# Performance work log

Hardware: AMD Instinct MI355X
Metric: run time of the kernel (lower is better)

## Reference

```python
import jax, jax.numpy as jnp
import numpy as np

B, C, H, W = 16, 64, 128, 128
C8 = C // 8


def setup_inputs() -> dict:
    key = jax.random.key(0)
    ks = jax.random.split(key, 8)
    s = 0.05
    return {
        "x": jax.random.normal(ks[0], (B, C, H, W), dtype=jnp.float32),
        "Wq": jax.random.normal(ks[1], (C8, C), dtype=jnp.float32) * s,
        "bq": jax.random.normal(ks[2], (C8,), dtype=jnp.float32) * s,
        "Wk": jax.random.normal(ks[3], (C8, C), dtype=jnp.float32) * s,
        "bk": jax.random.normal(ks[4], (C8,), dtype=jnp.float32) * s,
        "Wv": jax.random.normal(ks[5], (C, C), dtype=jnp.float32) * s,
        "bv": jax.random.normal(ks[6], (C,), dtype=jnp.float32) * s,
        "gamma": jnp.zeros((1,), dtype=jnp.float32),
    }


def _criss_cross(x, Wq, bq, Wk, bk, Wv, bv, gamma):
    # 1x1 convs == channel-mixing matmuls
    q = jnp.einsum("bchw,oc->bohw", x, Wq) + bq[None, :, None, None]  # [B,C8,H,W]
    k = jnp.einsum("bchw,oc->bohw", x, Wk) + bk[None, :, None, None]  # [B,C8,H,W]
    v = jnp.einsum("bchw,oc->bohw", x, Wv) + bv[None, :, None, None]  # [B,C,H,W]

    h = x.shape[2]
    # column (H-axis) attention scores; diagonal masked to -inf
    energy_H = jnp.einsum("bchw,bciw->bhwi", q, k)  # [B,H,W,H]
    diag = jnp.eye(h, dtype=bool)[None, :, None, :]  # mask where query row == key row
    energy_H = jnp.where(diag, -jnp.inf, energy_H)
    # row (W-axis) attention scores
    energy_W = jnp.einsum("bchw,bchj->bhwj", q, k)  # [B,H,W,W]

    # joint softmax over concatenated H+W axis
    att = jax.nn.softmax(jnp.concatenate([energy_H, energy_W], axis=3), axis=3)
    att_H = att[:, :, :, :h]    # [B,H,W,H]
    att_W = att[:, :, :, h:]    # [B,H,W,W]

    out_H = jnp.einsum("bhwi,bciw->bchw", att_H, v)
    out_W = jnp.einsum("bhwj,bchj->bchw", att_W, v)
    return gamma[0] * (out_H + out_W) + x


def reference(x, Wq, bq, Wk, bk, Wv, bv, gamma):
    return _criss_cross(x, Wq, bq, Wk, bk, Wv, bv, gamma)
```

## Files before the change

### kernel.cpp

```cpp
#include <hip/hip_runtime.h>

#define HW 128
#define CC 64
#define NB 16
#define LOG2E 1.44269504088896f

typedef _Float16 h1;
typedef _Float16 h2 __attribute__((ext_vector_type(2)));
typedef _Float16 half8 __attribute__((ext_vector_type(8)));
typedef float float16v __attribute__((ext_vector_type(16)));
typedef uint uv4 __attribute__((ext_vector_type(4)));

__device__ __forceinline__ uint packh2(float a, float b) {
#if __has_builtin(__builtin_amdgcn_cvt_pkrtz)
  return __builtin_bit_cast(uint, __builtin_amdgcn_cvt_pkrtz(a, b));
#else
  h2 v; v[0] = (h1)a; v[1] = (h1)b; return __builtin_bit_cast(uint, v);
#endif
}
__device__ __forceinline__ ushort f2h(float a) { h1 v = (h1)a; return __builtin_bit_cast(ushort, v); }
__device__ __forceinline__ float  h2f(ushort a) { return (float)__builtin_bit_cast(h1, a); }

__device__ __forceinline__ float fexp2(float x) {
#if __has_builtin(__builtin_amdgcn_exp2f)
  return __builtin_amdgcn_exp2f(x);
#else
  return exp2f(x);
#endif
}

__device__ __forceinline__ float16v mfma16(uv4 a, uv4 b, float16v c) {
  return __builtin_amdgcn_mfma_f32_32x32x16_f16(
      __builtin_bit_cast(half8, a), __builtin_bit_cast(half8, b), c, 0, 0, 0);
}

__global__ __launch_bounds__(256) void k_prep(
    const float* __restrict__ Wq, const float* __restrict__ bq,
    const float* __restrict__ Wk, const float* __restrict__ bk,
    const float* __restrict__ Wv, const float* __restrict__ bv,
    ushort* __restrict__ W_frag, float* __restrict__ bias_f)
{
  int idx = blockIdx.x * 256 + threadIdx.x;
  if (idx < 6144) {
    int g = idx >> 3, e = idx & 7;
    int kshi = g / 96, o = g % 96;
    int ks = kshi >> 1, hi = kshi & 1;
    int c = 8 * hi + 16 * ks + e;
    float val = (o < 8)  ? Wq[o * 64 + c] * LOG2E
              : (o < 16) ? Wk[(o - 8) * 64 + c]
              : (o < 80) ? Wv[(o - 16) * 64 + c] : 0.f;
    W_frag[idx] = f2h(val);
  }
  if (blockIdx.x == 0 && threadIdx.x < 96) {
    int t = threadIdx.x;
    bias_f[t] = (t < 8) ? bq[t] * LOG2E : (t < 16) ? bk[t - 8] : (t < 80) ? bv[t - 16] : 0.f;
  }
}

__global__ __launch_bounds__(256, 4) void k_projW(
    const float* __restrict__ x, const ushort* __restrict__ W_frag,
    const float* __restrict__ bias_f,
    ushort* __restrict__ qT, ushort* __restrict__ kT,
    ushort* __restrict__ v,
    ushort* __restrict__ oW_, float* __restrict__ mW_, float* __restrict__ sW_)
{
  alignas(16) __shared__ uint V_l[64 * 64];
  alignas(16) __shared__ ushort qk_l[128 * 24];
  __shared__ float bias_l[96];

  int t = threadIdx.x;
  int lane = t & 63, wv = t >> 6, hi = lane >> 5;
  int b = blockIdx.x >> 7, r = blockIdx.x & 127;
  if (t < 96) bias_l[t] = bias_f[t];

  int w = 32 * wv + (lane & 31);
  const float* xw = x + (size_t)(b * CC) * (HW * HW) + (size_t)r * HW + w;
  const size_t PL = (size_t)HW * HW;

  float xv[32];
  #pragma unroll
  for (int ks = 0; ks < 4; ++ks) {
    int c0 = 8 * hi + 16 * ks;
    #pragma unroll
    for (int e = 0; e < 8; ++e)
      xv[ks * 8 + e] = xw[(size_t)(c0 + e) * PL];
  }
  __syncthreads();

  float16v acc0 = {}, acc1 = {}, acc2 = {};
  #pragma unroll
  for (int ks = 0; ks < 4; ++ks) {
    uv4 Bx;
    #pragma unroll
    for (int e2 = 0; e2 < 4; ++e2)
      Bx[e2] = packh2(xv[ks * 8 + 2 * e2], xv[ks * 8 + 2 * e2 + 1]);
    const ushort* wf = W_frag + (size_t)(ks * 2 + hi) * 96 * 8;
    uv4 a0 = *(const uv4*)(wf + (lane & 31) * 8);
    uv4 a1 = *(const uv4*)(wf + ((lane & 31) + 32) * 8);
    uv4 a2 = *(const uv4*)(wf + ((lane & 31) + 64) * 8);
    acc0 = mfma16(a0, Bx, acc0);
    acc1 = mfma16(a1, Bx, acc1);
    acc2 = mfma16(a2, Bx, acc2);
  }

  #pragma unroll
  for (int reg = 0; reg < 16; ++reg) {
    int orow = (reg & 3) + 8 * (reg >> 2) + 4 * hi;
    float v0 = acc0[reg] + bias_l[orow];
    if (orow < 16) {
      qk_l[w * 24 + orow] = f2h(v0);
    } else {
      int c = orow - 16;
      *(ushort*)((char*)V_l + c * 256 + ((2 * w) ^ ((c & 15) << 4))) = f2h(v0);
    }
    int c1 = orow + 16;
    *(ushort*)((char*)V_l + c1 * 256 + ((2 * w) ^ ((c1 & 15) << 4))) =
        f2h(acc1[reg] + bias_l[orow + 32]);
    if (orow < 16) {
      int c2_ = orow + 48;
      *(ushort*)((char*)V_l + c2_ * 256 + ((2 * w) ^ ((c2_ & 15) << 4))) =
          f2h(acc2[reg] + bias_l[orow + 64]);
    }
  }
  __syncthreads();

  ushort* vb = v + (size_t)(b * CC) * PL + (size_t)r * HW;
  #pragma unroll
  for (int i = 0; i < 4; ++i) {
    int idx = t + 256 * i; int c = idx >> 4, j8 = idx & 15;
    uv4 val = *(const uv4*)((const char*)V_l + c * 256 + ((16 * j8) ^ ((c & 15) << 4)));
    *(uv4*)(vb + (size_t)c * PL + j8 * 8) = val;
  }
  {
    int pix = t & 127, isk = t >> 7;
    uv4 val = *(const uv4*)&qk_l[pix * 24 + isk * 8];
    ushort* dstt = (isk ? kT : qT) + ((size_t)(b * HW + pix) * HW + r) * 8;
    *(uv4*)dstt = val;
  }

  int qg = w;
  uv4 Bq = {0, 0, 0, 0};
  uv4 ka[4] = {{0,0,0,0}, {0,0,0,0}, {0,0,0,0}, {0,0,0,0}};
  if (hi == 0) {
    Bq = *(const uv4*)&qk_l[qg * 24];
    #pragma unroll
    for (int mt = 0; mt < 4; ++mt)
      ka[mt] = *(const uv4*)&qk_l[((lane & 31) + 32 * mt) * 24 + 8];
  }

  float16v e[4];
  #pragma unroll
  for (int mt = 0; mt < 4; ++mt) {
    float16v z = {};
    e[mt] = mfma16(ka[mt], Bq, z);
  }

  float m = -INFINITY;
  #pragma unroll
  for (int mt = 0; mt < 4; ++mt)
    #pragma unroll
    for (int reg = 0; reg < 16; reg += 2)
      m = fmaxf(m, fmaxf(e[mt][reg], e[mt][reg + 1]));
  m = fmaxf(m, __shfl_xor(m, 32));

  float s0 = 0.f, s1 = 0.f, s2 = 0.f, s3 = 0.f;
  #pragma unroll
  for (int mt = 0; mt < 4; ++mt) {
    #pragma unroll
    for (int reg = 0; reg < 16; reg += 4) {
      float p0 = fexp2(e[mt][reg + 0] - m);
      float p1 = fexp2(e[mt][reg + 1] - m);
      float p2 = fexp2(e[mt][reg + 2] - m);
      float p3 = fexp2(e[mt][reg + 3] - m);
      e[mt][reg + 0] = p0; e[mt][reg + 1] = p1;
      e[mt][reg + 2] = p2; e[mt][reg + 3] = p3;
      s0 += p0; s1 += p1; s2 += p2; s3 += p3;
    }
  }
  float s = (s0 + s1) + (s2 + s3);
  s += __shfl_xor(s, 32);
  if (lane < 32) {
    mW_[(size_t)blockIdx.x * HW + qg] = m;
    sW_[(size_t)blockIdx.x * HW + qg] = s;
  }

  float16v pacc0 = {}, pacc1 = {};
  #pragma unroll
  for (int s8 = 0; s8 < 8; ++s8) {
    int mt = s8 >> 1, hf = s8 & 1;
    float p0 = e[mt][8 * hf + 0], p1 = e[mt][8 * hf + 1];
    float p2 = e[mt][8 * hf + 2], p3 = e[mt][8 * hf + 3];
    float p4 = e[mt][8 * hf + 4], p5 = e[mt][8 * hf + 5];
    float p6 = e[mt][8 * hf + 6], p7 = e[mt][8 * hf + 7];
    uint X = packh2(p0, p1), Y = packh2(p2, p3), Z = packh2(p4, p5), Wp = packh2(p6, p7);
    uint Xs = __shfl_xor(X, 32), Ys = __shfl_xor(Y, 32);
    uint Zs = __shfl_xor(Z, 32), Ws = __shfl_xor(Wp, 32);
    uv4 Bp;
    Bp[0] = (hi == 0) ? X  : Zs;
    Bp[1] = (hi == 0) ? Y  : Ws;
    Bp[2] = (hi == 0) ? Xs : Z;
    Bp[3] = (hi == 0) ? Ys : Wp;
    #pragma unroll
    for (int ct = 0; ct < 2; ++ct) {
      int c = (lane & 31) + 32 * ct;
      uint byteoff = c * 256 + ((16 * (hi + 2 * s8)) ^ ((c & 15) << 4));
      uv4 va = *(const uv4*)((const char*)V_l + byteoff);
      if (ct == 0) pacc0 = mfma16(va, Bp, pacc0);
      else         pacc1 = mfma16(va, Bp, pacc1);
    }
  }

  __syncthreads();
  ushort* o_l = (ushort*)V_l;
  #pragma unroll
  for (int reg = 0; reg < 16; ++reg) {
    int c = (reg & 3) + 8 * (reg >> 2) + 4 * hi;
    o_l[(c +  0) * 128 + w] = f2h(pacc0[reg]);
    o_l[(c + 32) * 128 + w] = f2h(pacc1[reg]);
  }
  __syncthreads();
  ushort* ob = oW_ + (size_t)(b * CC) * PL + (size_t)r * HW;
  #pragma unroll
  for (int i = 0; i < 4; ++i) {
    int idx = t + 256 * i; int c = idx >> 4, w8 = idx & 15;
    *(uv4*)(ob + (size_t)c * PL + w8 * 8) = *(const uv4*)&o_l[c * 128 + w8 * 8];
  }
}

__global__ __launch_bounds__(256) void k_transpose_v(const ushort* __restrict__ v,
                                                     ushort* __restrict__ vT)
{
  __shared__ ushort tl[128 * 130];
  int t = threadIdx.x;
  size_t base = (size_t)blockIdx.x * (HW * HW);
  const uint* ip = (const uint*)(v + base);
  uint* op = (uint*)(vT + base);
  int c2 = t & 63;
  int r0 = t >> 6;
  for (int it = 0; it < 32; ++it) {
    int r = it * 4 + r0;
    uint val = ip[r * 64 + c2];
    *(uint*)&tl[r * 130 + c2 * 2] = val;
  }
  __syncthreads();
  for (int it = 0; it < 32; ++it) {
    int wcol = it * 4 + r0;
    int hh = c2 * 2;
    uint lo = tl[hh * 130 + wcol];
    uint hi = tl[(hh + 1) * 130 + wcol];
    op[wcol * 64 + c2] = lo | (hi << 16);
  }
}

__global__ __launch_bounds__(256, 4) void k_attnH(
    const ushort* __restrict__ qT, const ushort* __restrict__ kT,
    const ushort* __restrict__ vT,
    const float* __restrict__ mW_, const float* __restrict__ sW_,
    ushort* __restrict__ oH_, ushort* __restrict__ aWn)
{
  alignas(16) __shared__ uint V_l[64 * 64];

  int t = threadIdx.x;
  int lane = t & 63, wv = t >> 6;
  int hi = lane >> 5;
  int bid = blockIdx.x;
  int b = bid >> 7, r = bid & 127;
  size_t plane32 = (size_t)(HW * HW) / 2;
  const size_t PL = (size_t)HW * HW;
  size_t pixbase = (size_t)(b * HW + r) * HW * 8;

  int qg = 32 * wv + (lane & 31);
  uv4 Bq = {0, 0, 0, 0};
  uv4 ka[4] = {{0,0,0,0}, {0,0,0,0}, {0,0,0,0}, {0,0,0,0}};
  if (hi == 0) {
    Bq = *(const uv4*)(qT + pixbase + (size_t)qg * 8);
    #pragma unroll
    for (int mt = 0; mt < 4; ++mt)
      ka[mt] = *(const uv4*)(kT + pixbase + (size_t)((lane & 31) + 32 * mt) * 8);
  }
  float mw = mW_[(size_t)b * PL + (size_t)qg * HW + r];
  float sw = sW_[(size_t)b * PL + (size_t)qg * HW + r];

  const uint* vrow = (const uint*)vT + (size_t)(b * CC) * plane32 + (size_t)r * 64;
  #pragma unroll
  for (int i = 0; i < 4; ++i) {
    int idx = t + 256 * i; int c = idx >> 4, j4 = idx & 15;
    uv4 val = *(const uv4*)(vrow + (size_t)c * plane32 + 4 * j4);
    uint byteoff = c * 256 + ((16 * j4) ^ ((c & 15) << 4));
    *(uv4*)((char*)V_l + byteoff) = val;
  }
  __syncthreads();

  float16v e[4];
  #pragma unroll
  for (int mt = 0; mt < 4; ++mt) {
    float16v z = {};
    e[mt] = mfma16(ka[mt], Bq, z);
  }

  #pragma unroll
  for (int mt = 0; mt < 4; ++mt)
    #pragma unroll
    for (int reg = 0; reg < 16; ++reg) {
      int key = 32 * mt + ((reg & 3) + 8 * (reg >> 2) + 4 * hi);
      e[mt][reg] = (key == qg) ? -INFINITY : e[mt][reg];
    }

  float m = -INFINITY;
  #pragma unroll
  for (int mt = 0; mt < 4; ++mt)
    #pragma unroll
    for (int reg = 0; reg < 16; reg += 2)
      m = fmaxf(m, fmaxf(e[mt][reg], e[mt][reg + 1]));
  m = fmaxf(m, __shfl_xor(m, 32));

  float s0 = 0.f, s1 = 0.f, s2 = 0.f, s3 = 0.f;
  #pragma unroll
  for (int mt = 0; mt < 4; ++mt) {
    #pragma unroll
    for (int reg = 0; reg < 16; reg += 4) {
      float p0 = fexp2(e[mt][reg + 0] - m);
      float p1 = fexp2(e[mt][reg + 1] - m);
      float p2 = fexp2(e[mt][reg + 2] - m);
      float p3 = fexp2(e[mt][reg + 3] - m);
      e[mt][reg + 0] = p0; e[mt][reg + 1] = p1;
      e[mt][reg + 2] = p2; e[mt][reg + 3] = p3;
      s0 += p0; s1 += p1; s2 += p2; s3 += p3;
    }
  }
  float s = (s0 + s1) + (s2 + s3);
  s += __shfl_xor(s, 32);

  float mm = fmaxf(m, mw);
  float eh = fexp2(m - mm), ew = fexp2(mw - mm);
  float inv = 1.f / (s * eh + sw * ew);
  float aH = eh * inv;
  if (hi == 0)
    aWn[(size_t)b * PL + (size_t)qg * HW + r] = f2h(ew * inv);

  float16v acc0 = {}, acc1 = {};
  #pragma unroll
  for (int s8 = 0; s8 < 8; ++s8) {
    int mt = s8 >> 1, hf = s8 & 1;
    float p0 = e[mt][8 * hf + 0], p1 = e[mt][8 * hf + 1];
    float p2 = e[mt][8 * hf + 2], p3 = e[mt][8 * hf + 3];
    float p4 = e[mt][8 * hf + 4], p5 = e[mt][8 * hf + 5];
    float p6 = e[mt][8 * hf + 6], p7 = e[mt][8 * hf + 7];
    uint X = packh2(p0, p1), Y = packh2(p2, p3), Z = packh2(p4, p5), Wp = packh2(p6, p7);
    uint Xs = __shfl_xor(X, 32), Ys = __shfl_xor(Y, 32);
    uint Zs = __shfl_xor(Z, 32), Ws = __shfl_xor(Wp, 32);
    uv4 Bp;
    Bp[0] = (hi == 0) ? X  : Zs;
    Bp[1] = (hi == 0) ? Y  : Ws;
    Bp[2] = (hi == 0) ? Xs : Z;
    Bp[3] = (hi == 0) ? Ys : Wp;
    #pragma unroll
    for (int ct = 0; ct < 2; ++ct) {
      int c = (lane & 31) + 32 * ct;
      uint byteoff = c * 256 + ((16 * (hi + 2 * s8)) ^ ((c & 15) << 4));
      uv4 va = *(const uv4*)((const char*)V_l + byteoff);
      if (ct == 0) acc0 = mfma16(va, Bp, acc0);
      else         acc1 = mfma16(va, Bp, acc1);
    }
  }

  __syncthreads();
  ushort* o_l = (ushort*)V_l;
  int w = 32 * wv + (lane & 31);
  #pragma unroll
  for (int reg = 0; reg < 16; ++reg) {
    int c = (reg & 3) + 8 * (reg >> 2) + 4 * hi;
    o_l[(c +  0) * 128 + w] = f2h(acc0[reg] * aH);
    o_l[(c + 32) * 128 + w] = f2h(acc1[reg] * aH);
  }
  __syncthreads();
  ushort* ob = oH_ + (size_t)(b * CC) * PL + (size_t)r * HW;
  #pragma unroll
  for (int i = 0; i < 4; ++i) {
    int idx = t + 256 * i; int c = idx >> 4, w8 = idx & 15;
    *(uv4*)(ob + (size_t)c * PL + w8 * 8) = *(const uv4*)&o_l[c * 128 + w8 * 8];
  }
}

__global__ __launch_bounds__(256) void k_merge(
    const ushort* __restrict__ oHT, const ushort* __restrict__ oW,
    const ushort* __restrict__ aWn,
    const float* __restrict__ x, const float* __restrict__ gamma,
    float* __restrict__ out)
{
  alignas(16) __shared__ ushort otile[2 * 32 * 132];
  int t = threadIdx.x;
  int bid = blockIdx.x;
  int wsel = bid & 3, cg = (bid >> 2) & 31, b = bid >> 7;
  int w0 = wsel * 32;
  float g = gamma[0];
  const int PL = HW * HW;

  uv4 ov[4];
  #pragma unroll
  for (int i = 0; i < 4; ++i) {
    int p = t + 256 * i;
    int ch = p >> 9, rest = p & 511;
    int w = rest >> 4, hg = rest & 15;
    size_t cbase = (size_t)(b * CC + cg * 2 + ch) * PL;
    ov[i] = *(const uv4*)(oHT + cbase + (size_t)(w0 + w) * HW + hg * 8);
  }
  uint2 owp[8]; float4 xp[8]; uint2 awp[4];
  #pragma unroll
  for (int i = 0; i < 2; ++i) {
    int p = t + 256 * i;
    int w4 = p & 7, hh2 = p >> 3;
    #pragma unroll
    for (int rr = 0; rr < 2; ++rr) {
      int hh = 2 * hh2 + rr;
      size_t poff = (size_t)hh * HW + w0 + 4 * w4;
      awp[i * 2 + rr] = *(const uint2*)(aWn + (size_t)b * PL + poff);
      #pragma unroll
      for (int ch = 0; ch < 2; ++ch) {
        size_t base = (size_t)(b * CC + cg * 2 + ch) * PL + poff;
        owp[ch * 4 + i * 2 + rr] = *(const uint2*)(oW + base);
        xp[ch * 4 + i * 2 + rr]  = *(const float4*)(x + base);
      }
    }
  }
  #pragma unroll
  for (int i = 0; i < 4; ++i) {
    int p = t + 256 * i;
    int ch = p >> 9, rest = p & 511;
    int w = rest >> 4, hg = rest & 15;
    *(uv4*)&otile[(ch * 32 + w) * 132 + hg * 8] = ov[i];
  }
  __syncthreads();

  #pragma unroll
  for (int ch = 0; ch < 2; ++ch) {
    size_t cbase = (size_t)(b * CC + cg * 2 + ch) * PL;
    const ushort* otc = &otile[ch * 32 * 132];
    #pragma unroll
    for (int i = 0; i < 2; ++i) {
      int p = t + 256 * i;
      int w4 = p & 7, hh2 = p >> 3;
      float th0[4], th1[4];
      #pragma unroll
      for (int j = 0; j < 4; ++j) {
        uint pk = *(const uint*)&otc[(4 * w4 + j) * 132 + 2 * hh2];
        th0[j] = h2f((ushort)(pk & 0xffff));
        th1[j] = h2f((ushort)(pk >> 16));
      }
      #pragma unroll
      for (int rr = 0; rr < 2; ++rr) {
        int hh = 2 * hh2 + rr;
        const float* th = rr ? th1 : th0;
        size_t base = cbase + (size_t)hh * HW + w0 + 4 * w4;
        uint2 aw2 = awp[i * 2 + rr];
        uint2 ow2 = owp[ch * 4 + i * 2 + rr];
        float4 xv = xp[ch * 4 + i * 2 + rr];
        float4 res;
        res.x = g * (th[0] + h2f((ushort)(ow2.x & 0xffff)) * h2f((ushort)(aw2.x & 0xffff))) + xv.x;
        res.y = g * (th[1] + h2f((ushort)(ow2.x >> 16))    * h2f((ushort)(aw2.x >> 16)))    + xv.y;
        res.z = g * (th[2] + h2f((ushort)(ow2.y & 0xffff)) * h2f((ushort)(aw2.y & 0xffff))) + xv.z;
        res.w = g * (th[3] + h2f((ushort)(ow2.y >> 16))    * h2f((ushort)(aw2.y >> 16)))    + xv.w;
        *(float4*)(out + base) = res;
      }
    }
  }
}

extern "C" void kernel_launch(void* const* d_in, const int* in_sizes, int n_in,
                              void* d_out, int out_size, void* d_ws, size_t ws_size,
                              hipStream_t stream)
{
  const float* x     = (const float*)d_in[0];
  const float* Wq    = (const float*)d_in[1];
  const float* bq    = (const float*)d_in[2];
  const float* Wk    = (const float*)d_in[3];
  const float* bk    = (const float*)d_in[4];
  const float* Wv    = (const float*)d_in[5];
  const float* bv    = (const float*)d_in[6];
  const float* gamma = (const float*)d_in[7];
  float* out = (float*)d_out;

  char* w = (char*)d_ws;
  size_t np = (size_t)NB * HW * HW;
  ushort* W_frag = (ushort*)w; w += 6144 * 2;
  float*  bias_f = (float*)w;  w += 96 * 4 + 320;
  ushort* qT  = (ushort*)w;  w += np * 8 * 2;
  ushort* kT  = (ushort*)w;  w += np * 8 * 2;
  ushort* v   = (ushort*)w;  w += np * CC * 2;
  ushort* vT  = (ushort*)w;  w += np * CC * 2;
  ushort* oW  = (ushort*)w;  w += np * CC * 2;
  ushort* oHT = (ushort*)w;  w += np * CC * 2;
  float* mW = (float*)w;  w += np * 4;
  float* sW = (float*)w;  w += np * 4;
  ushort* aWn = (ushort*)w; w += np * 2;
  if ((size_t)(w - (char*)d_ws) > ws_size) return;

  k_prep<<<24, 256, 0, stream>>>(Wq, bq, Wk, bk, Wv, bv, W_frag, bias_f);
  k_projW<<<NB * HW, 256, 0, stream>>>(x, W_frag, bias_f, qT, kT, v, oW, mW, sW);
  k_transpose_v<<<NB * CC, 256, 0, stream>>>(v, vT);
  k_attnH<<<NB * HW, 256, 0, stream>>>(qT, kT, vT, mW, sW, oHT, aWn);
  k_merge<<<NB * 32 * 4, 256, 0, stream>>>(oHT, oW, aWn, x, gamma, out);
}
```

Measured before the change: 104.8 us.

## Process two rows per projW block and prefetch next row's x during compute

k_projW now handles two consecutive rows per block, launching half as many blocks. The x loads for the second row are issued after the first row's LDS staging, so their global-memory latency overlaps with the first row's stores, attention and output. In exchange, register pressure rises from holding a second 32-float x buffer, which may hurt occupancy under launch_bounds(256,4), and the grid has fewer blocks.

Result: slower. 162.0 us (+54.5%).

```diff
diff --git a/kernel.cpp b/kernel.cpp
--- a/kernel.cpp
+++ b/kernel.cpp
@@ -70,83 +70,249 @@
 
   int t = threadIdx.x;
   int lane = t & 63, wv = t >> 6, hi = lane >> 5;
-  int b = blockIdx.x >> 7, r = blockIdx.x & 127;
+  int b = blockIdx.x >> 6, r0 = (blockIdx.x & 63) << 1;
   if (t < 96) bias_l[t] = bias_f[t];
 
   int w = 32 * wv + (lane & 31);
-  const float* xw = x + (size_t)(b * CC) * (HW * HW) + (size_t)r * HW + w;
   const size_t PL = (size_t)HW * HW;
-
-  float xv[32];
-  #pragma unroll
-  for (int ks = 0; ks < 4; ++ks) {
-    int c0 = 8 * hi + 16 * ks;
-    #pragma unroll
-    for (int e = 0; e < 8; ++e)
-      xv[ks * 8 + e] = xw[(size_t)(c0 + e) * PL];
+  const float* xbase = x + (size_t)(b * CC) * PL + w;
+
+  float xv[32], xv2[32];
+  {
+    const float* xw = xbase + (size_t)r0 * HW;
+    #pragma unroll
+    for (int ks = 0; ks < 4; ++ks) {
+      int c0 = 8 * hi + 16 * ks;
+      #pragma unroll
+      for (int e = 0; e < 8; ++e)
+        xv[ks * 8 + e] = xw[(size_t)(c0 + e) * PL];
+    }
+  }
+
+  for (int rr = 0; rr < 2; ++rr) {
+    int r = r0 + rr;
+
+    float16v acc0 = {}, acc1 = {}, acc2 = {};
+    #pragma unroll
+    for (int ks = 0; ks < 4; ++ks) {
+      uv4 Bx;
+      #pragma unroll
+      for (int e2 = 0; e2 < 4; ++e2)
+        Bx[e2] = packh2(xv[ks * 8 + 2 * e2], xv[ks * 8 + 2 * e2 + 1]);
+      const ushort* wf = W_frag + (size_t)(ks * 2 + hi) * 96 * 8;
+      uv4 a0 = *(const uv4*)(wf + (lane & 31) * 8);
+      uv4 a1 = *(const uv4*)(wf + ((lane & 31) + 32) * 8);
+      uv4 a2 = *(const uv4*)(wf + ((lane & 31) + 64) * 8);
+      acc0 = mfma16(a0, Bx, acc0);
+      acc1 = mfma16(a1, Bx, acc1);
+      acc2 = mfma16(a2, Bx, acc2);
+    }
+    __syncthreads();
+
+    #pragma unroll
+    for (int reg = 0; reg < 16; ++reg) {
+      int orow = (reg & 3) + 8 * (reg >> 2) + 4 * hi;
+      float v0 = acc0[reg] + bias_l[orow];
+      if (orow < 16) {
+        qk_l[w * 24 + orow] = f2h(v0);
+      } else {
+        int c = orow - 16;
+        *(ushort*)((char*)V_l + c * 256 + ((2 * w) ^ ((c & 15) << 4))) = f2h(v0);
+      }
+      int c1 = orow + 16;
+      *(ushort*)((char*)V_l + c1 * 256 + ((2 * w) ^ ((c1 & 15) << 4))) =
+          f2h(acc1[reg] + bias_l[orow + 32]);
+      if (orow < 16) {
+        int c2_ = orow + 48;
+        *(ushort*)((char*)V_l + c2_ * 256 + ((2 * w) ^ ((c2_ & 15) << 4))) =
+            f2h(acc2[reg] + bias_l[orow + 64]);
+      }
+    }
+    __syncthreads();
+
+    if (rr == 0) {
+      const float* xw = xbase + (size_t)(r0 + 1) * HW;
+      #pragma unroll
+      for (int ks = 0; ks < 4; ++ks) {
+        int c0 = 8 * hi + 16 * ks;
+        #pragma unroll
+        for (int e = 0; e < 8; ++e)
+          xv2[ks * 8 + e] = xw[(size_t)(c0 + e) * PL];
+      }
+    }
+
+    ushort* vb = v + (size_t)(b * CC) * PL + (size_t)r * HW;
+    #pragma unroll
+    for (int i = 0; i < 4; ++i) {
+      int idx = t + 256 * i; int c = idx >> 4, j8 = idx & 15;
+      uv4 val = *(const uv4*)((const char*)V_l + c * 256 + ((16 * j8) ^ ((c & 15) << 4)));
+      *(uv4*)(vb + (size_t)c * PL + j8 * 8) = val;
+    }
+    {
+      int pix = t & 127, isk = t >> 7;
+      uv4 val = *(const uv4*)&qk_l[pix * 24 + isk * 8];
+      ushort* dstt = (isk ? kT : qT) + ((size_t)(b * HW + pix) * HW + r) * 8;
+      *(uv4*)dstt = val;
+    }
+
+    int qg = w;
+    uv4 Bq = {0, 0, 0, 0};
+    uv4 ka[4] = {{0,0,0,0}, {0,0,0,0}, {0,0,0,0}, {0,0,0,0}};
+    if (hi == 0) {
+      Bq = *(const uv4*)&qk_l[qg * 24];
+      #pragma unroll
+      for (int mt = 0; mt < 4; ++mt)
+        ka[mt] = *(const uv4*)&qk_l[((lane & 31) + 32 * mt) * 24 + 8];
+    }
+
+    float16v e[4];
+    #pragma unroll
+    for (int mt = 0; mt < 4; ++mt) {
+      float16v z = {};
+      e[mt] = mfma16(ka[mt], Bq, z);
+    }
+
+    float m = -INFINITY;
+    #pragma unroll
+    for (int mt = 0; mt < 4; ++mt)
+      #pragma unroll
+      for (int reg = 0; reg < 16; reg += 2)
+        m = fmaxf(m, fmaxf(e[mt][reg], e[mt][reg + 1]));
+    m = fmaxf(m, __shfl_xor(m, 32));
+
+    float s0 = 0.f, s1 = 0.f, s2 = 0.f, s3 = 0.f;
+    #pragma unroll
+    for (int mt = 0; mt < 4; ++mt) {
+      #pragma unroll
+      for (int reg = 0; reg < 16; reg += 4) {
+        float p0 = fexp2(e[mt][reg + 0] - m);
+        float p1 = fexp2(e[mt][reg + 1] - m);
+        float p2 = fexp2(e[mt][reg + 2] - m);
+        float p3 = fexp2(e[mt][reg + 3] - m);
+        e[mt][reg + 0] = p0; e[mt][reg + 1] = p1;
+        e[mt][reg + 2] = p2; e[mt][reg + 3] = p3;
+        s0 += p0; s1 += p1; s2 += p2; s3 += p3;
+      }
+    }
+    float s = (s0 + s1) + (s2 + s3);
+    s += __shfl_xor(s, 32);
+    if (lane < 32) {
+      mW_[((size_t)(b * HW + r)) * HW + qg] = m;
+      sW_[((size_t)(b * HW + r)) * HW + qg] = s;
+    }
+
+    float16v pacc0 = {}, pacc1 = {};
+    #pragma unroll
+    for (int s8 = 0; s8 < 8; ++s8) {
+      int mt = s8 >> 1, hf = s8 & 1;
+      float p0 = e[mt][8 * hf + 0], p1 = e[mt][8 * hf + 1];
+      float p2 = e[mt][8 * hf + 2], p3 = e[mt][8 * hf + 3];
+      float p4 = e[mt][8 * hf + 4], p5 = e[mt][8 * hf + 5];
+      float p6 = e[mt][8 * hf + 6], p7 = e[mt][8 * hf + 7];
+      uint X = packh2(p0, p1), Y = packh2(p2, p3), Z = packh2(p4, p5), Wp = packh2(p6, p7);
+      uint Xs = __shfl_xor(X, 32), Ys = __shfl_xor(Y, 32);
+      uint Zs = __shfl_xor(Z, 32), Ws = __shfl_xor(Wp, 32);
+      uv4 Bp;
+      Bp[0] = (hi == 0) ? X  : Zs;
+      Bp[1] = (hi == 0) ? Y  : Ws;
+      Bp[2] = (hi == 0) ? Xs : Z;
+      Bp[3] = (hi == 0) ? Ys : Wp;
+      #pragma unroll
+      for (int ct = 0; ct < 2; ++ct) {
+        int c = (lane & 31) + 32 * ct;
+        uint byteoff = c * 256 + ((16 * (hi + 2 * s8)) ^ ((c & 15) << 4));
+        uv4 va = *(const uv4*)((const char*)V_l + byteoff);
+        if (ct == 0) pacc0 = mfma16(va, Bp, pacc0);
+        else         pacc1 = mfma16(va, Bp, pacc1);
+      }
+    }
+
+    __syncthreads();
+    ushort* o_l = (ushort*)V_l;
+    #pragma unroll
+    for (int reg = 0; reg < 16; ++reg) {
+      int c = (reg & 3) + 8 * (reg >> 2) + 4 * hi;
+      o_l[(c +  0) * 128 + w] = f2h(pacc0[reg]);
+      o_l[(c + 32) * 128 + w] = f2h(pacc1[reg]);
+    }
+    __syncthreads();
+    ushort* ob = oW_ + (size_t)(b * CC) * PL + (size_t)r * HW;
+    #pragma unroll
+    for (int i = 0; i < 4; ++i) {
+      int idx = t + 256 * i; int c = idx >> 4, w8 = idx & 15;
+      *(uv4*)(ob + (size_t)c * PL + w8 * 8) = *(const uv4*)&o_l[c * 128 + w8 * 8];
+    }
+
+    if (rr == 0) {
+      #pragma unroll
+      for (int i = 0; i < 32; ++i) xv[i] = xv2[i];
+    }
+  }
+}
+
+__global__ __launch_bounds__(256) void k_transpose_v(const ushort* __restrict__ v,
+                                                     ushort* __restrict__ vT)
+{
+  __shared__ ushort tl[128 * 130];
+  int t = threadIdx.x;
+  size_t base = (size_t)blockIdx.x * (HW * HW);
+  const uint* ip = (const uint*)(v + base);
+  uint* op = (uint*)(vT + base);
+  int c2 = t & 63;
+  int r0 = t >> 6;
+  for (int it = 0; it < 32; ++it) {
+    int r = it * 4 + r0;
+    uint val = ip[r * 64 + c2];
+    *(uint*)&tl[r * 130 + c2 * 2] = val;
   }
   __syncthreads();
-
-  float16v acc0 = {}, acc1 = {}, acc2 = {};
-  #pragma unroll
-  for (int ks = 0; ks < 4; ++ks) {
-    uv4 Bx;
-    #pragma unroll
-    for (int e2 = 0; e2 < 4; ++e2)
-      Bx[e2] = packh2(xv[ks * 8 + 2 * e2], xv[ks * 8 + 2 * e2 + 1]);
-    const ushort* wf = W_frag + (size_t)(ks * 2 + hi) * 96 * 8;
-    uv4 a0 = *(const uv4*)(wf + (lane & 31) * 8);
-    uv4 a1 = *(const uv4*)(wf + ((lane & 31) + 32) * 8);
-    uv4 a2 = *(const uv4*)(wf + ((lane & 31) + 64) * 8);
-    acc0 = mfma16(a0, Bx, acc0);
-    acc1 = mfma16(a1, Bx, acc1);
-    acc2 = mfma16(a2, Bx, acc2);
-  }
-
-  #pragma unroll
-  for (int reg = 0; reg < 16; ++reg) {
-    int orow = (reg & 3) + 8 * (reg >> 2) + 4 * hi;
-    float v0 = acc0[reg] + bias_l[orow];
-    if (orow < 16) {
-      qk_l[w * 24 + orow] = f2h(v0);
-    } else {
-      int c = orow - 16;
-      *(ushort*)((char*)V_l + c * 256 + ((2 * w) ^ ((c & 15) << 4))) = f2h(v0);
-    }
-    int c1 = orow + 16;
-    *(ushort*)((char*)V_l + c1 * 256 + ((2 * w) ^ ((c1 & 15) << 4))) =
-        f2h(acc1[reg] + bias_l[orow + 32]);
-    if (orow < 16) {
-      int c2_ = orow + 48;
-      *(ushort*)((char*)V_l + c2_ * 256 + ((2 * w) ^ ((c2_ & 15) << 4))) =
-          f2h(acc2[reg] + bias_l[orow + 64]);
-    }
-  }
-  __syncthreads();
-
-  ushort* vb = v + (size_t)(b * CC) * PL + (size_t)r * HW;
-  #pragma unroll
-  for (int i = 0; i < 4; ++i) {
-    int idx = t + 256 * i; int c = idx >> 4, j8 = idx & 15;
-    uv4 val = *(const uv4*)((const char*)V_l + c * 256 + ((16 * j8) ^ ((c & 15) << 4)));
-    *(uv4*)(vb + (size_t)c * PL + j8 * 8) = val;
-  }
-  {
-    int pix = t & 127, isk = t >> 7;
-    uv4 val = *(const uv4*)&qk_l[pix * 24 + isk * 8];
-    ushort* dstt = (isk ? kT : qT) + ((size_t)(b * HW + pix) * HW + r) * 8;
-    *(uv4*)dstt = val;
-  }
-
-  int qg = w;
+  for (int it = 0; it < 32; ++it) {
+    int wcol = it * 4 + r0;
+    int hh = c2 * 2;
+    uint lo = tl[hh * 130 + wcol];
+    uint hi = tl[(hh + 1) * 130 + wcol];
+    op[wcol * 64 + c2] = lo | (hi << 16);
+  }
+}
+
+__global__ __launch_bounds__(256, 4) void k_attnH(
+    const ushort* __restrict__ qT, const ushort* __restrict__ kT,
+    const ushort* __restrict__ vT,
+    const float* __restrict__ mW_, const float* __restrict__ sW_,
+    ushort* __restrict__ oH_, ushort* __restrict__ aWn)
+{
+  alignas(16) __shared__ uint V_l[64 * 64];
+
+  int t = threadIdx.x;
+  int lane = t & 63, wv = t >> 6;
+  int hi = lane >> 5;
+  int bid = blockIdx.x;
+  int b = bid >> 7, r = bid & 127;
+  size_t plane32 = (size_t)(HW * HW) / 2;
+  const size_t PL = (size_t)HW * HW;
+  size_t pixbase = (size_t)(b * HW + r) * HW * 8;
+
+  int qg = 32 * wv + (lane & 31);
   uv4 Bq = {0, 0, 0, 0};
   uv4 ka[4] = {{0,0,0,0}, {0,0,0,0}, {0,0,0,0}, {0,0,0,0}};
   if (hi == 0) {
-    Bq = *(const uv4*)&qk_l[qg * 24];
+    Bq = *(const uv4*)(qT + pixbase + (size_t)qg * 8);
     #pragma unroll
     for (int mt = 0; mt < 4; ++mt)
-      ka[mt] = *(const uv4*)&qk_l[((lane & 31) + 32 * mt) * 24 + 8];
-  }
+      ka[mt] = *(const uv4*)(kT + pixbase + (size_t)((lane & 31) + 32 * mt) * 8);
+  }
+  float mw = mW_[(size_t)b * PL + (size_t)qg * HW + r];
+  float sw = sW_[(size_t)b * PL + (size_t)qg * HW + r];
+
+  const uint* vrow = (const uint*)vT + (size_t)(b * CC) * plane32 + (size_t)r * 64;
+  #pragma unroll
+  for (int i = 0; i < 4; ++i) {
+    int idx = t + 256 * i; int c = idx >> 4, j4 = idx & 15;
+    uv4 val = *(const uv4*)(vrow + (size_t)c * plane32 + 4 * j4);
+    uint byteoff = c * 256 + ((16 * j4) ^ ((c & 15) << 4));
+    *(uv4*)((char*)V_l + byteoff) = val;
+  }
+  __syncthreads();
 
   float16v e[4];
   #pragma unroll
@@ -154,6 +320,14 @@
     float16v z = {};
     e[mt] = mfma16(ka[mt], Bq, z);
   }
+
+  #pragma unroll
+  for (int mt = 0; mt < 4; ++mt)
+    #pragma unroll
+    for (int reg = 0; reg < 16; ++reg) {
+      int key = 32 * mt + ((reg & 3) + 8 * (reg >> 2) + 4 * hi);
+      e[mt][reg] = (key == qg) ? -INFINITY : e[mt][reg];
+    }
 
   float m = -INFINITY;
   #pragma unroll
@@ -179,12 +353,15 @@
   }
   float s = (s0 + s1) + (s2 + s3);
   s += __shfl_xor(s, 32);
-  if (lane < 32) {
-    mW_[(size_t)blockIdx.x * HW + qg] = m;
-    sW_[(size_t)blockIdx.x * HW + qg] = s;
-  }
-
-  float16v pacc0 = {}, pacc1 = {};
+
+  float mm = fmaxf(m, mw);
+  float eh = fexp2(m - mm), ew = fexp2(mw - mm);
+  float inv = 1.f / (s * eh + sw * ew);
+  float aH = eh * inv;
+  if (hi == 0)
+    aWn[(size_t)b * PL + (size_t)qg * HW + r] = f2h(ew * inv);
+
+  float16v acc0 = {}, acc1 = {};
   #pragma unroll
   for (int s8 = 0; s8 < 8; ++s8) {
     int mt = s8 >> 1, hf = s8 & 1;
@@ -205,160 +382,6 @@
       int c = (lane & 31) + 32 * ct;
       uint byteoff = c * 256 + ((16 * (hi + 2 * s8)) ^ ((c & 15) << 4));
       uv4 va = *(const uv4*)((const char*)V_l + byteoff);
-      if (ct == 0) pacc0 = mfma16(va, Bp, pacc0);
-      else         pacc1 = mfma16(va, Bp, pacc1);
-    }
-  }
-
-  __syncthreads();
-  ushort* o_l = (ushort*)V_l;
-  #pragma unroll
-  for (int reg = 0; reg < 16; ++reg) {
-    int c = (reg & 3) + 8 * (reg >> 2) + 4 * hi;
-    o_l[(c +  0) * 128 + w] = f2h(pacc0[reg]);
-    o_l[(c + 32) * 128 + w] = f2h(pacc1[reg]);
-  }
-  __syncthreads();
-  ushort* ob = oW_ + (size_t)(b * CC) * PL + (size_t)r * HW;
-  #pragma unroll
-  for (int i = 0; i < 4; ++i) {
-    int idx = t + 256 * i; int c = idx >> 4, w8 = idx & 15;
-    *(uv4*)(ob + (size_t)c * PL + w8 * 8) = *(const uv4*)&o_l[c * 128 + w8 * 8];
-  }
-}
-
-__global__ __launch_bounds__(256) void k_transpose_v(const ushort* __restrict__ v,
-                                                     ushort* __restrict__ vT)
-{
-  __shared__ ushort tl[128 * 130];
-  int t = threadIdx.x;
-  size_t base = (size_t)blockIdx.x * (HW * HW);
-  const uint* ip = (const uint*)(v + base);
-  uint* op = (uint*)(vT + base);
-  int c2 = t & 63;
-  int r0 = t >> 6;
-  for (int it = 0; it < 32; ++it) {
-    int r = it * 4 + r0;
-    uint val = ip[r * 64 + c2];
-    *(uint*)&tl[r * 130 + c2 * 2] = val;
-  }
-  __syncthreads();
-  for (int it = 0; it < 32; ++it) {
-    int wcol = it * 4 + r0;
-    int hh = c2 * 2;
-    uint lo = tl[hh * 130 + wcol];
-    uint hi = tl[(hh + 1) * 130 + wcol];
-    op[wcol * 64 + c2] = lo | (hi << 16);
-  }
-}
-
-__global__ __launch_bounds__(256, 4) void k_attnH(
-    const ushort* __restrict__ qT, const ushort* __restrict__ kT,
-    const ushort* __restrict__ vT,
-    const float* __restrict__ mW_, const float* __restrict__ sW_,
-    ushort* __restrict__ oH_, ushort* __restrict__ aWn)
-{
-  alignas(16) __shared__ uint V_l[64 * 64];
-
-  int t = threadIdx.x;
-  int lane = t & 63, wv = t >> 6;
-  int hi = lane >> 5;
-  int bid = blockIdx.x;
-  int b = bid >> 7, r = bid & 127;
-  size_t plane32 = (size_t)(HW * HW) / 2;
-  const size_t PL = (size_t)HW * HW;
-  size_t pixbase = (size_t)(b * HW + r) * HW * 8;
-
-  int qg = 32 * wv + (lane & 31);
-  uv4 Bq = {0, 0, 0, 0};
-  uv4 ka[4] = {{0,0,0,0}, {0,0,0,0}, {0,0,0,0}, {0,0,0,0}};
-  if (hi == 0) {
-    Bq = *(const uv4*)(qT + pixbase + (size_t)qg * 8);
-    #pragma unroll
-    for (int mt = 0; mt < 4; ++mt)
-      ka[mt] = *(const uv4*)(kT + pixbase + (size_t)((lane & 31) + 32 * mt) * 8);
-  }
-  float mw = mW_[(size_t)b * PL + (size_t)qg * HW + r];
-  float sw = sW_[(size_t)b * PL + (size_t)qg * HW + r];
-
-  const uint* vrow = (const uint*)vT + (size_t)(b * CC) * plane32 + (size_t)r * 64;
-  #pragma unroll
-  for (int i = 0; i < 4; ++i) {
-    int idx = t + 256 * i; int c = idx >> 4, j4 = idx & 15;
-    uv4 val = *(const uv4*)(vrow + (size_t)c * plane32 + 4 * j4);
-    uint byteoff = c * 256 + ((16 * j4) ^ ((c & 15) << 4));
-    *(uv4*)((char*)V_l + byteoff) = val;
-  }
-  __syncthreads();
-
-  float16v e[4];
-  #pragma unroll
-  for (int mt = 0; mt < 4; ++mt) {
-    float16v z = {};
-    e[mt] = mfma16(ka[mt], Bq, z);
-  }
-
-  #pragma unroll
-  for (int mt = 0; mt < 4; ++mt)
-    #pragma unroll
-    for (int reg = 0; reg < 16; ++reg) {
-      int key = 32 * mt + ((reg & 3) + 8 * (reg >> 2) + 4 * hi);
-      e[mt][reg] = (key == qg) ? -INFINITY : e[mt][reg];
-    }
-
-  float m = -INFINITY;
-  #pragma unroll
-  for (int mt = 0; mt < 4; ++mt)
-    #pragma unroll
-    for (int reg = 0; reg < 16; reg += 2)
-      m = fmaxf(m, fmaxf(e[mt][reg], e[mt][reg + 1]));
-  m = fmaxf(m, __shfl_xor(m, 32));
-
-  float s0 = 0.f, s1 = 0.f, s2 = 0.f, s3 = 0.f;
-  #pragma unroll
-  for (int mt = 0; mt < 4; ++mt) {
-    #pragma unroll
-    for (int reg = 0; reg < 16; reg += 4) {
-      float p0 = fexp2(e[mt][reg + 0] - m);
-      float p1 = fexp2(e[mt][reg + 1] - m);
-      float p2 = fexp2(e[mt][reg + 2] - m);
-      float p3 = fexp2(e[mt][reg + 3] - m);
-      e[mt][reg + 0] = p0; e[mt][reg + 1] = p1;
-      e[mt][reg + 2] = p2; e[mt][reg + 3] = p3;
-      s0 += p0; s1 += p1; s2 += p2; s3 += p3;
-    }
-  }
-  float s = (s0 + s1) + (s2 + s3);
-  s += __shfl_xor(s, 32);
-
-  float mm = fmaxf(m, mw);
-  float eh = fexp2(m - mm), ew = fexp2(mw - mm);
-  float inv = 1.f / (s * eh + sw * ew);
-  float aH = eh * inv;
-  if (hi == 0)
-    aWn[(size_t)b * PL + (size_t)qg * HW + r] = f2h(ew * inv);
-
-  float16v acc0 = {}, acc1 = {};
-  #pragma unroll
-  for (int s8 = 0; s8 < 8; ++s8) {
-    int mt = s8 >> 1, hf = s8 & 1;
-    float p0 = e[mt][8 * hf + 0], p1 = e[mt][8 * hf + 1];
-    float p2 = e[mt][8 * hf + 2], p3 = e[mt][8 * hf + 3];
-    float p4 = e[mt][8 * hf + 4], p5 = e[mt][8 * hf + 5];
-    float p6 = e[mt][8 * hf + 6], p7 = e[mt][8 * hf + 7];
-    uint X = packh2(p0, p1), Y = packh2(p2, p3), Z = packh2(p4, p5), Wp = packh2(p6, p7);
-    uint Xs = __shfl_xor(X, 32), Ys = __shfl_xor(Y, 32);
-    uint Zs = __shfl_xor(Z, 32), Ws = __shfl_xor(Wp, 32);
-    uv4 Bp;
-    Bp[0] = (hi == 0) ? X  : Zs;
-    Bp[1] = (hi == 0) ? Y  : Ws;
-    Bp[2] = (hi == 0) ? Xs : Z;
-    Bp[3] = (hi == 0) ? Ys : Wp;
-    #pragma unroll
-    for (int ct = 0; ct < 2; ++ct) {
-      int c = (lane & 31) + 32 * ct;
-      uint byteoff = c * 256 + ((16 * (hi + 2 * s8)) ^ ((c & 15) << 4));
-      uv4 va = *(const uv4*)((const char*)V_l + byteoff);
       if (ct == 0) acc0 = mfma16(va, Bp, acc0);
       else         acc1 = mfma16(va, Bp, acc1);
     }
@@ -496,7 +519,7 @@
   if ((size_t)(w - (char*)d_ws) > ws_size) return;
 
   k_prep<<<24, 256, 0, stream>>>(Wq, bq, Wk, bk, Wv, bv, W_frag, bias_f);
-  k_projW<<<NB * HW, 256, 0, stream>>>(x, W_frag, bias_f, qT, kT, v, oW, mW, sW);
+  k_projW<<<NB * 64, 256, 0, stream>>>(x, W_frag, bias_f, qT, kT, v, oW, mW, sW);
   k_transpose_v<<<NB * CC, 256, 0, stream>>>(v, vT);
   k_attnH<<<NB * HW, 256, 0, stream>>>(qT, kT, vT, mW, sW, oHT, aWn);
   k_merge<<<NB * 32 * 4, 256, 0, stream>>>(oHT, oW, aWn, x, gamma, out);
```
